# Kernel optimization log

Measured on AMD Instinct MI355X. Metric: run time of the kernel, lower is better.

Reference implementation:

```python
import jax, jax.numpy as jnp
import numpy as np

N = 100000          # nodes
C_IN = 128          # incoming clusters (mask columns)
F = 116             # n_feature (e.g. AAL atlas ROIs)
N_CLUSTER = 64      # output clusters
EPS_BN = 1e-5
EPS_CORR = 1e-12


def setup_inputs() -> dict:
    key = jax.random.key(0)
    ks = jax.random.split(key, 8)
    inp = {
        "x_cov": jax.random.normal(ks[0], (N, F, F), dtype=jnp.float32),
        "mask_labels": jax.random.randint(ks[1], (N,), 0, C_IN, dtype=jnp.int32),
        "gumbel_u": jax.random.uniform(ks[2], (C_IN, N_CLUSTER), dtype=jnp.float32),
        "w1": jax.random.normal(ks[3], (256, F), dtype=jnp.float32) / np.sqrt(F),
        "b1": jnp.zeros((256,), dtype=jnp.float32),
        "g1": jnp.ones((F,), dtype=jnp.float32),
        "be1": jnp.zeros((F,), dtype=jnp.float32),
        "w2": jax.random.normal(ks[4], (N_CLUSTER, 256), dtype=jnp.float32) / np.sqrt(256.0),
        "b2": jnp.zeros((N_CLUSTER,), dtype=jnp.float32),
        "g2": jnp.ones((256,), dtype=jnp.float32),
        "be2": jnp.zeros((256,), dtype=jnp.float32),
    }
    return inp


def _batch_norm(x, g, b):
    # BatchNorm1d in training mode: batch stats, biased variance
    mu = x.mean(axis=0)
    var = x.var(axis=0)
    return g * (x - mu) * jax.lax.rsqrt(var + EPS_BN) + b


def _correlation_readout(cov):
    # cov: [C, F, F] -> correlation matrix, then row-mean readout -> [C, F]
    d = jnp.sqrt(jnp.clip(jnp.diagonal(cov, axis1=1, axis2=2), 0.0))  # [C, F]
    corr = cov / (d[:, :, None] * d[:, None, :] + EPS_CORR)
    return corr.mean(axis=-1)


def reference(x_cov, mask_labels, gumbel_u, w1, b1, g1, be1, w2, b2, g2, be2):
    # sparse.mm(mask.T, x_cov.reshape(-1, F*F)) == segment-sum of node covs per cluster
    flat = x_cov.reshape(-1, F * F)                                   # [N, F*F]
    cov = jax.ops.segment_sum(flat, mask_labels, num_segments=C_IN)   # [C_in, F*F]
    cov = cov.reshape(-1, F, F)                                       # [C_in, F, F]

    x_corr = _correlation_readout(cov)                                # [C_in, F]

    # MLP: bn -> lin -> relu -> bn -> lin
    h = jax.nn.relu(_batch_norm(x_corr, g1, be1) @ w1.T + b1)         # [C_in, 256]
    logits = _batch_norm(h, g2, be2) @ w2.T + b2                      # [C_in, n_cluster]

    # hard gumbel-softmax, tau=1, dim=1, straight-through
    u = jnp.clip(gumbel_u, 1e-6, 1.0 - 1e-6)
    gumbels = -jnp.log(-jnp.log(u))
    y_soft = jax.nn.softmax(logits + gumbels, axis=1)
    y_hard = jax.nn.one_hot(jnp.argmax(y_soft, axis=1), N_CLUSTER, dtype=y_soft.dtype)
    mask_out = y_hard - jax.lax.stop_gradient(y_soft) + y_soft        # [C_in, n_cluster]

    return cov, x_corr, mask_out
```

## Files before the change

### kernel.cpp

```cpp
#include <hip/hip_runtime.h>

#define N_NODES 100000
#define C_IN    128
#define F       116
#define FF      (F * F)
#define H1      256
#define NCL     64
#define EPS_BN   1e-5f
#define EPS_CORR 1e-12f

#define NBLK 256
#define NPB  ((N_NODES + NBLK - 1) / NBLK)


__global__ __launch_bounds__(256) void k_hist(const int* __restrict__ lab,
                                              int* __restrict__ blkhist) {
    __shared__ int lh[C_IN];
    const int b = blockIdx.x, t = threadIdx.x;
    if (t < C_IN) lh[t] = 0;
    __syncthreads();
    const int s = b * NPB;
    int e = s + NPB; if (e > N_NODES) e = N_NODES;
    for (int n = s + t; n < e; n += 256)
        atomicAdd(&lh[lab[n]], 1);
    __syncthreads();
    if (t < C_IN) blkhist[b * C_IN + t] = lh[t];
}

__global__ __launch_bounds__(128) void k_scan(const int* __restrict__ blkhist,
                                              int* __restrict__ blkoff,
                                              int* __restrict__ coff) {
    __shared__ int tot[C_IN];
    const int l = threadIdx.x;
    int run = 0;
    for (int b = 0; b < NBLK; ++b) {
        int v = blkhist[b * C_IN + l];
        blkoff[b * C_IN + l] = run;
        run += v;
    }
    const int mine = run;
    tot[l] = run;
    __syncthreads();
    for (int d = 1; d < C_IN; d <<= 1) {
        int v = (l >= d) ? tot[l - d] : 0;
        __syncthreads();
        tot[l] += v;
        __syncthreads();
    }
    coff[l] = tot[l] - mine;
    if (l == C_IN - 1) coff[C_IN] = tot[l];
}

__global__ __launch_bounds__(256) void k_scatter(const int* __restrict__ lab,
                                                 const int* __restrict__ blkoff,
                                                 const int* __restrict__ coff,
                                                 unsigned* __restrict__ bucket) {
    __shared__ int cur[C_IN];
    const int b = blockIdx.x, t = threadIdx.x;
    if (t < C_IN) cur[t] = coff[t] + blkoff[b * C_IN + t];
    __syncthreads();
    const int s = b * NPB;
    int e = s + NPB; if (e > N_NODES) e = N_NODES;
    for (int n = s + t; n < e; n += 256) {
        int l = lab[n];
        int pos = atomicAdd(&cur[l], 1);
        bucket[pos] = (unsigned)n * (unsigned)FF;
    }
}


__global__ __launch_bounds__(256) void k_segsum(const float* __restrict__ x,
                                                const unsigned* __restrict__ bucket,
                                                const int* __restrict__ coff,
                                                float* __restrict__ cov) {
    const int label = blockIdx.y;
    const int col   = blockIdx.x * 256 + threadIdx.x;
    const bool valid = col < (FF / 4);
    const int j4 = (valid ? col : (FF / 4 - 1)) * 4;

    const int beg = coff[label];
    const int end = coff[label + 1];

    __shared__ unsigned nd[1024];
    float4 a0acc = make_float4(0.f, 0.f, 0.f, 0.f);
    float4 a1acc = make_float4(0.f, 0.f, 0.f, 0.f);

    for (int base = beg; base < end; base += 1024) {
        int cl = end - base;
        if (cl > 1024) cl = 1024;
        __syncthreads();
        for (int i = threadIdx.x; i < cl; i += 256)
            nd[i] = bucket[base + i];
        __syncthreads();

        int i = 0;
        for (; i + 4 <= cl; i += 4) {
            const float4 v0 = *(const float4*)(x + (size_t)nd[i]     + j4);
            const float4 v1 = *(const float4*)(x + (size_t)nd[i + 1] + j4);
            const float4 v2 = *(const float4*)(x + (size_t)nd[i + 2] + j4);
            const float4 v3 = *(const float4*)(x + (size_t)nd[i + 3] + j4);
            a0acc.x += v0.x; a0acc.y += v0.y; a0acc.z += v0.z; a0acc.w += v0.w;
            a1acc.x += v1.x; a1acc.y += v1.y; a1acc.z += v1.z; a1acc.w += v1.w;
            a0acc.x += v2.x; a0acc.y += v2.y; a0acc.z += v2.z; a0acc.w += v2.w;
            a1acc.x += v3.x; a1acc.y += v3.y; a1acc.z += v3.z; a1acc.w += v3.w;
        }
        for (; i < cl; ++i) {
            const float4 v = *(const float4*)(x + (size_t)nd[i] + j4);
            a0acc.x += v.x; a0acc.y += v.y; a0acc.z += v.z; a0acc.w += v.w;
        }
    }

    if (valid) {
        float4 r;
        r.x = a0acc.x + a1acc.x; r.y = a0acc.y + a1acc.y;
        r.z = a0acc.z + a1acc.z; r.w = a0acc.w + a1acc.w;
        *(float4*)(cov + (size_t)label * FF + j4) = r;
    }
}


__global__ __launch_bounds__(128) void k_corr(const float* __restrict__ cov,
                                              float* __restrict__ xcorr) {
    const int c = blockIdx.x;
    const float* Cm = cov + (size_t)c * FF;
    __shared__ float d[F];
    const int t = threadIdx.x;
    if (t < F) d[t] = sqrtf(fmaxf(Cm[t * F + t], 0.f));
    __syncthreads();
    if (t < F) {
        const float di = d[t];
        float s = 0.f;
        for (int j = 0; j < F; ++j)
            s += Cm[t * F + j] / (di * d[j] + EPS_CORR);
        xcorr[c * F + t] = s / (float)F;
    }
}


__global__ __launch_bounds__(256) void k_mm1(const float* __restrict__ xcorr,
                                             const float* __restrict__ g1,
                                             const float* __restrict__ be1,
                                             const float* __restrict__ w1,
                                             const float* __restrict__ b1,
                                             float* __restrict__ h) {
    const int c = blockIdx.x;
    const int t = threadIdx.x;
    __shared__ float xb[F];
    if (t < F) {
        float s = 0.f;
        for (int cc = 0; cc < C_IN; ++cc) s += xcorr[cc * F + t];
        const float m = s / (float)C_IN;
        float v = 0.f;
        for (int cc = 0; cc < C_IN; ++cc) {
            const float dd = xcorr[cc * F + t] - m;
            v += dd * dd;
        }
        v /= (float)C_IN;
        xb[t] = g1[t] * (xcorr[c * F + t] - m) * rsqrtf(v + EPS_BN) + be1[t];
    }
    __syncthreads();
    float acc = b1[t];
    const float* wr = w1 + t * F;
    for (int f = 0; f < F; ++f) acc += xb[f] * wr[f];
    h[c * H1 + t] = fmaxf(acc, 0.f);
}

__global__ __launch_bounds__(256) void k_mm2(const float* __restrict__ h,
                                             const float* __restrict__ g2,
                                             const float* __restrict__ be2,
                                             const float* __restrict__ w2,
                                             const float* __restrict__ b2,
                                             const float* __restrict__ gu,
                                             float* __restrict__ mask) {
    const int c = blockIdx.x;
    const int t = threadIdx.x;
    __shared__ float hb[H1];
    __shared__ float part[4][NCL];

    {
        float s = 0.f;
        for (int cc = 0; cc < C_IN; ++cc) s += h[cc * H1 + t];
        const float m = s / (float)C_IN;
        float v = 0.f;
        for (int cc = 0; cc < C_IN; ++cc) {
            const float dd = h[cc * H1 + t] - m;
            v += dd * dd;
        }
        v /= (float)C_IN;
        hb[t] = g2[t] * (h[c * H1 + t] - m) * rsqrtf(v + EPS_BN) + be2[t];
    }
    __syncthreads();

    const int k = t & 63, p = t >> 6;
    float acc = 0.f;
    const float* wr = w2 + k * H1 + p * 64;
    const float* hp = hb + p * 64;
    for (int o = 0; o < 64; ++o) acc += hp[o] * wr[o];
    part[p][k] = acc;
    __syncthreads();

    if (t < NCL) {
        float z = b2[t] + part[0][t] + part[1][t] + part[2][t] + part[3][t];
        float u = gu[c * NCL + t];
        u = fminf(fmaxf(u, 1e-6f), 1.f - 1e-6f);
        z = z - logf(-logf(u));

        float m = z;
        for (int d = 32; d; d >>= 1) m = fmaxf(m, __shfl_xor(m, d));
        const float e = expf(z - m);
        float s = e;
        for (int d = 32; d; d >>= 1) s += __shfl_xor(s, d);
        const float y = e / s;

        float bv = z; int bi = t;
        for (int d = 32; d; d >>= 1) {
            float ov = __shfl_xor(bv, d);
            int   oi = __shfl_xor(bi, d);
            if (ov > bv || (ov == bv && oi < bi)) { bv = ov; bi = oi; }
        }
        const float hard = (t == bi) ? 1.f : 0.f;
        mask[c * NCL + t] = (hard - y) + y;
    }
}


extern "C" void kernel_launch(void* const* d_in, const int* in_sizes, int n_in,
                              void* d_out, int out_size, void* d_ws, size_t ws_size,
                              hipStream_t stream) {
    const float* x_cov = (const float*)d_in[0];
    const int*   lab   = (const int*)d_in[1];
    const float* gu    = (const float*)d_in[2];
    const float* w1    = (const float*)d_in[3];
    const float* b1    = (const float*)d_in[4];
    const float* g1    = (const float*)d_in[5];
    const float* be1   = (const float*)d_in[6];
    const float* w2    = (const float*)d_in[7];
    const float* b2    = (const float*)d_in[8];
    const float* g2    = (const float*)d_in[9];
    const float* be2   = (const float*)d_in[10];

    float* cov_out   = (float*)d_out;
    float* xcorr_out = cov_out + (size_t)C_IN * FF;
    float* mask_out  = xcorr_out + (size_t)C_IN * F;

    int*      blkhist = (int*)d_ws;
    int*      blkoff  = blkhist + NBLK * C_IN;
    int*      coff    = blkoff + NBLK * C_IN;
    unsigned* bucket  = (unsigned*)(coff + 132);
    float*    h       = (float*)(bucket + N_NODES);

    k_hist   <<<NBLK, 256, 0, stream>>>(lab, blkhist);
    k_scan   <<<1, 128, 0, stream>>>(blkhist, blkoff, coff);
    k_scatter<<<NBLK, 256, 0, stream>>>(lab, blkoff, coff, bucket);

    k_segsum <<<dim3(14, C_IN), 256, 0, stream>>>(x_cov, bucket, coff, cov_out);

    k_corr   <<<C_IN, 128, 0, stream>>>(cov_out, xcorr_out);
    k_mm1    <<<C_IN, 256, 0, stream>>>(xcorr_out, g1, be1, w1, b1, h);
    k_mm2    <<<C_IN, 256, 0, stream>>>(h, g2, be2, w2, b2, gu, mask_out);
}
```

Measured before the change: 966.5 us.

## Use nontemporal loads in segsum, stage scan in LDS, fewer hist blocks, rcp in corr

The segment-sum kernel now reads the node covariance matrices with nontemporal vector loads, so the single-use stream bypasses cache retention. The block count for the histogram and scatter passes is halved. The scan kernel stages the per-block histogram in shared memory before its serial walk. The correlation kernel replaces the division with a hardware reciprocal, which changes rounding slightly. The main cost targeted is the roughly 5.4 GB gather in segsum; the other edits trim small kernels.

```diff
diff --git a/kernel.cpp b/kernel.cpp
--- a/kernel.cpp
+++ b/kernel.cpp
@@ -9,8 +9,10 @@
 #define EPS_BN   1e-5f
 #define EPS_CORR 1e-12f
 
-#define NBLK 256
+#define NBLK 128
 #define NPB  ((N_NODES + NBLK - 1) / NBLK)
+
+typedef float f32x4 __attribute__((ext_vector_type(4)));
 
 
 __global__ __launch_bounds__(256) void k_hist(const int* __restrict__ lab,
@@ -30,12 +32,15 @@
 __global__ __launch_bounds__(128) void k_scan(const int* __restrict__ blkhist,
                                               int* __restrict__ blkoff,
                                               int* __restrict__ coff) {
+    __shared__ int hl[NBLK * C_IN];
     __shared__ int tot[C_IN];
     const int l = threadIdx.x;
+    for (int i = l; i < NBLK * C_IN; i += 128) hl[i] = blkhist[i];
+    __syncthreads();
     int run = 0;
     for (int b = 0; b < NBLK; ++b) {
-        int v = blkhist[b * C_IN + l];
-        blkoff[b * C_IN + l] = run;
+        int v = hl[b * C_IN + l];
+        hl[b * C_IN + l] = run;
         run += v;
     }
     const int mine = run;
@@ -49,6 +54,8 @@
     }
     coff[l] = tot[l] - mine;
     if (l == C_IN - 1) coff[C_IN] = tot[l];
+    __syncthreads();
+    for (int i = l; i < NBLK * C_IN; i += 128) blkoff[i] = hl[i];
 }
 
 __global__ __launch_bounds__(256) void k_scatter(const int* __restrict__ lab,
@@ -82,8 +89,8 @@
     const int end = coff[label + 1];
 
     __shared__ unsigned nd[1024];
-    float4 a0acc = make_float4(0.f, 0.f, 0.f, 0.f);
-    float4 a1acc = make_float4(0.f, 0.f, 0.f, 0.f);
+    f32x4 acc0 = (f32x4)(0.f);
+    f32x4 acc1 = (f32x4)(0.f);
 
     for (int base = beg; base < end; base += 1024) {
         int cl = end - base;
@@ -95,26 +102,21 @@
 
         int i = 0;
         for (; i + 4 <= cl; i += 4) {
-            const float4 v0 = *(const float4*)(x + (size_t)nd[i]     + j4);
-            const float4 v1 = *(const float4*)(x + (size_t)nd[i + 1] + j4);
-            const float4 v2 = *(const float4*)(x + (size_t)nd[i + 2] + j4);
-            const float4 v3 = *(const float4*)(x + (size_t)nd[i + 3] + j4);
-            a0acc.x += v0.x; a0acc.y += v0.y; a0acc.z += v0.z; a0acc.w += v0.w;
-            a1acc.x += v1.x; a1acc.y += v1.y; a1acc.z += v1.z; a1acc.w += v1.w;
-            a0acc.x += v2.x; a0acc.y += v2.y; a0acc.z += v2.z; a0acc.w += v2.w;
-            a1acc.x += v3.x; a1acc.y += v3.y; a1acc.z += v3.z; a1acc.w += v3.w;
+            const f32x4 v0 = __builtin_nontemporal_load((const f32x4*)(x + (size_t)nd[i]     + j4));
+            const f32x4 v1 = __builtin_nontemporal_load((const f32x4*)(x + (size_t)nd[i + 1] + j4));
+            const f32x4 v2 = __builtin_nontemporal_load((const f32x4*)(x + (size_t)nd[i + 2] + j4));
+            const f32x4 v3 = __builtin_nontemporal_load((const f32x4*)(x + (size_t)nd[i + 3] + j4));
+            acc0 += v0; acc1 += v1; acc0 += v2; acc1 += v3;
         }
         for (; i < cl; ++i) {
-            const float4 v = *(const float4*)(x + (size_t)nd[i] + j4);
-            a0acc.x += v.x; a0acc.y += v.y; a0acc.z += v.z; a0acc.w += v.w;
+            const f32x4 v = __builtin_nontemporal_load((const f32x4*)(x + (size_t)nd[i] + j4));
+            acc0 += v;
         }
     }
 
     if (valid) {
-        float4 r;
-        r.x = a0acc.x + a1acc.x; r.y = a0acc.y + a1acc.y;
-        r.z = a0acc.z + a1acc.z; r.w = a0acc.w + a1acc.w;
-        *(float4*)(cov + (size_t)label * FF + j4) = r;
+        const f32x4 r = acc0 + acc1;
+        *(f32x4*)(cov + (size_t)label * FF + j4) = r;
     }
 }
 
@@ -131,8 +133,8 @@
         const float di = d[t];
         float s = 0.f;
         for (int j = 0; j < F; ++j)
-            s += Cm[t * F + j] / (di * d[j] + EPS_CORR);
-        xcorr[c * F + t] = s / (float)F;
+            s += Cm[t * F + j] * __builtin_amdgcn_rcpf(di * d[j] + EPS_CORR);
+        xcorr[c * F + t] = s * (1.f / (float)F);
     }
 }
 
```

Measured after the change: 891.7 us. 7.7% less time.
